# Optimization experiments

Hardware: AMD Instinct MI355X
Metric: run time of the kernel (lower is better)

Reference implementation:

```python
import jax, jax.numpy as jnp
import numpy as np

DIMS = 1024
HEADS = 16
HEAD_DIM = DIMS // HEADS


def setup_inputs() -> dict:
    key = jax.random.key(0)
    k_x, k_q, k_k, k_v = jax.random.split(key, 4)
    scale = 1.0 / np.sqrt(DIMS)
    return {
        "input_seq_embs": jax.random.normal(k_x, (4, 4096, DIMS), dtype=jnp.float32),
        # torch nn.Linear weights have shape (out_features, in_features)
        "W_Q": jax.random.normal(k_q, (DIMS, DIMS), dtype=jnp.float32) * scale,
        "W_K": jax.random.normal(k_k, (DIMS, DIMS), dtype=jnp.float32) * scale,
        "W_V": jax.random.normal(k_v, (DIMS, DIMS), dtype=jnp.float32) * scale,
    }


def reference(input_seq_embs, W_Q, W_K, W_V):
    B, L, d = input_seq_embs.shape
    H, hd = HEADS, HEAD_DIM
    # torch Linear: y = x @ W.T
    Q = (input_seq_embs @ W_Q.T).reshape(B, L, H, hd)
    K = (input_seq_embs @ W_K.T).reshape(B, L, H, hd)
    V = (input_seq_embs @ W_V.T).reshape(B, L, H, hd)
    # NOTE: original code does NOT move heads to dim 1, so matmuls act on
    # the trailing (H, hd) axes per token.
    # softmax(K^T) over heads axis: (B, L, hd, H)
    sK = jax.nn.softmax(jnp.swapaxes(K, -1, -2), axis=-1)
    # tran_V: (B, L, hd, hd)
    tran_V = jnp.einsum("bldh,blhe->blde", sK, V)
    # softmax(Q) over head_dim axis, then (B, L, H, hd)
    out = jnp.einsum("blhd,blde->blhe", jax.nn.softmax(Q, axis=-1), tran_V)
    return out.reshape(B, L, d)
```

## Files before the change

### kernel.cpp

```cpp
#include <hip/hip_runtime.h>
#include <stdint.h>
#include <stddef.h>

#define TOKENS 16384
#define CHUNK  8192
#define DMODEL 1024

typedef short   short8 __attribute__((ext_vector_type(8)));
typedef _Float16 half8 __attribute__((ext_vector_type(8)));
typedef float   f32x4  __attribute__((ext_vector_type(4)));
typedef unsigned short ushort_t;
typedef unsigned short us4 __attribute__((ext_vector_type(4)));

__device__ inline ushort_t f2h(float f) {
  union { _Float16 h; ushort_t u; } x; x.h = (_Float16)f; return x.u;
}
__device__ inline float h2f(ushort_t u) {
  union { _Float16 h; ushort_t u; } x; x.u = u; return (float)x.h;
}

template <typename V>
__device__ auto mfma16h_(V a, V b, f32x4 c, int)
    -> decltype(__builtin_amdgcn_mfma_f32_16x16x32_f16(a, b, c, 0, 0, 0)) {
  return __builtin_amdgcn_mfma_f32_16x16x32_f16(a, b, c, 0, 0, 0);
}
template <typename V>
__device__ f32x4 mfma16h_(V a, V b, f32x4 c, long) {
  return __builtin_amdgcn_mfma_f32_16x16x32_f16(
      __builtin_bit_cast(half8, a), __builtin_bit_cast(half8, b), c, 0, 0, 0);
}
__device__ inline f32x4 MFMA16H(short8 a, short8 b, f32x4 c) {
  return mfma16h_(a, b, c, 0);
}

__device__ inline void gload_lds16(const void* g, void* l) {
  __builtin_amdgcn_global_load_lds(
      (const __attribute__((address_space(1))) unsigned int*)g,
      (__attribute__((address_space(3))) unsigned int*)l, 16, 0, 0);
}

__device__ inline void wave_lds_fence() {
  asm volatile("s_waitcnt lgkmcnt(0)" ::: "memory");
  __builtin_amdgcn_sched_barrier(0);
}

__global__ __launch_bounds__(256) void conv_w(
    const float* __restrict__ Wq, const float* __restrict__ Wk,
    const float* __restrict__ Wv, ushort_t* __restrict__ Wh, int n4)
{
  int i = blockIdx.x * 256 + threadIdx.x;
  if (i >= n4) return;
  const float* src = (blockIdx.y == 0) ? Wq : ((blockIdx.y == 1) ? Wk : Wv);
  f32x4 x = ((const f32x4*)src)[i];
  us4 h;
  #pragma unroll
  for (int j = 0; j < 4; ++j) h[j] = f2h(x[j]);
  ((us4*)(Wh + (size_t)blockIdx.y * DMODEL * DMODEL))[i] = h;
}

__global__ __launch_bounds__(256) void conv_x(
    const float* __restrict__ src, ushort_t* __restrict__ dst, int n4)
{
  int i = blockIdx.x * 256 + threadIdx.x;
  if (i >= n4) return;
  f32x4 x = ((const f32x4*)src)[i];
  us4 h;
  #pragma unroll
  for (int j = 0; j < 4; ++j) h[j] = f2h(x[j]);
  ((us4*)dst)[i] = h;
}

__global__ __launch_bounds__(512, 2) void gemm_h(
    const ushort_t* __restrict__ Xh, const ushort_t* __restrict__ Wh,
    ushort_t* __restrict__ Y, int tokens)
{
  __shared__ ushort_t As[2][256 * 64];
  __shared__ ushort_t Bs[2][256 * 64];

  const int tid  = threadIdx.x;
  const int lane = tid & 63;
  const int wid  = tid >> 6;
  const int quad = lane >> 4;
  const int l15  = lane & 15;
  const int wm   = wid >> 2;
  const int wn   = wid & 3;

  const int m0 = blockIdx.x * 256;
  const int n0 = blockIdx.y * 256;
  const int z  = blockIdx.z;

  const ushort_t* Ag = Xh + (size_t)m0 * DMODEL;
  const ushort_t* Bg = Wh + (size_t)z * DMODEL * DMODEL + (size_t)n0 * DMODEL;
  ushort_t* Yp = Y + (size_t)z * tokens * DMODEL;

  f32x4 acc[8][4] = {};

  auto stageA = [&](int t, int b) {
    const int kbase = t * 64;
    #pragma unroll
    for (int i = 0; i < 4; ++i) {
      const int c    = i * 512 + tid;
      const int row  = c >> 3;
      const int koff = (((c & 7) ^ (row & 7)) << 3);
      gload_lds16(Ag + (size_t)row * DMODEL + kbase + koff,
                  (char*)As[b] + (i * 512 + wid * 64) * 16);
    }
  };
  auto stageB = [&](int t, int b) {
    const int kbase = t * 64;
    #pragma unroll
    for (int i = 0; i < 4; ++i) {
      const int c    = i * 512 + tid;
      const int row  = c >> 3;
      const int koff = (((c & 7) ^ (row & 7)) << 3);
      gload_lds16(Bg + (size_t)row * DMODEL + kbase + koff,
                  (char*)Bs[b] + (i * 512 + wid * 64) * 16);
    }
  };

  stageA(0, 0);
  stageB(0, 0);
  asm volatile("s_waitcnt vmcnt(0)" ::: "memory");
  __syncthreads();

  for (int t = 0; t < DMODEL / 64; ++t) {
    const int b  = t & 1;
    const bool pf = (t + 1 < DMODEL / 64);
    const short8* Av = (const short8*)As[b];
    const short8* Bv = (const short8*)Bs[b];

    short8 bh[4][2];
    #pragma unroll
    for (int j = 0; j < 4; ++j) {
      const int r = wn * 64 + j * 16 + l15;
      #pragma unroll
      for (int s = 0; s < 2; ++s)
        bh[j][s] = Bv[r * 8 + ((s * 4 + quad) ^ (r & 7))];
    }

    #pragma unroll
    for (int p = 0; p < 4; ++p) {
      short8 ah[2][2];
      #pragma unroll
      for (int ii = 0; ii < 2; ++ii) {
        const int r = wm * 128 + (2 * p + ii) * 16 + l15;
        #pragma unroll
        for (int s = 0; s < 2; ++s)
          ah[ii][s] = Av[r * 8 + ((s * 4 + quad) ^ (r & 7))];
      }
      if (p == 0 && pf) stageA(t + 1, b ^ 1);
      if (p == 1 && pf) stageB(t + 1, b ^ 1);

      __builtin_amdgcn_s_barrier();
      asm volatile("s_waitcnt lgkmcnt(0)" ::: "memory");
      __builtin_amdgcn_sched_barrier(0);
      __builtin_amdgcn_s_setprio(1);
      #pragma unroll
      for (int s = 0; s < 2; ++s) {
        #pragma unroll
        for (int ii = 0; ii < 2; ++ii) {
          #pragma unroll
          for (int j = 0; j < 4; ++j)
            acc[2 * p + ii][j] = MFMA16H(ah[ii][s], bh[j][s], acc[2 * p + ii][j]);
        }
      }
      __builtin_amdgcn_s_setprio(0);
      __builtin_amdgcn_s_barrier();
    }

    if (pf) { asm volatile("s_waitcnt vmcnt(0)" ::: "memory"); }
    __syncthreads();
  }

  #pragma unroll
  for (int i = 0; i < 8; ++i) {
    #pragma unroll
    for (int j = 0; j < 4; ++j) {
      #pragma unroll
      for (int r = 0; r < 4; ++r) {
        int row = m0 + wm * 128 + i * 16 + quad * 4 + r;
        int col = n0 + wn * 64 + j * 16 + l15;
        Yp[(size_t)row * DMODEL + col] = f2h(acc[i][j][r]);
      }
    }
  }
}

__global__ __launch_bounds__(256) void attn_mix(
    const ushort_t* __restrict__ QKV, float* __restrict__ Out, int tokens)
{
  __shared__ __align__(16) ushort_t V_s[4][16 * 72];
  __shared__ __align__(16) float    M_s[4][16 * 20];

  const int tid  = threadIdx.x;
  const int lane = tid & 63;
  const int wv   = tid >> 6;
  const int tok  = blockIdx.x * 4 + wv;

  const int l15  = lane & 15;
  const int quad = lane >> 4;
  const int hrow = lane >> 3;
  const int dcol = (lane & 7) * 8;

  ushort_t* Vl = V_s[wv];
  float*    Ml = M_s[wv];

  const size_t base = (size_t)tok * DMODEL;
  const size_t zstr = (size_t)tokens * DMODEL;
  const short8* Q8 = (const short8*)(QKV + base);
  const short8* K8 = (const short8*)(QKV + zstr + base);
  const short8* V8 = (const short8*)(QKV + 2 * zstr + base);

  short8 vra = V8[lane], vrb = V8[64 + lane];
  *(short8*)(Vl + hrow * 72 + dcol)       = vra;
  *(short8*)(Vl + (hrow + 8) * 72 + dcol) = vrb;

  const int fidx = l15 * 8 + quad;
  short8 qf0 = Q8[fidx], qf1 = Q8[fidx + 4];
  short8 kf0 = K8[fidx], kf1 = K8[fidx + 4];

  float eq0[8], eq1[8], ek0[8], ek1[8];
  #pragma unroll
  for (int j = 0; j < 8; ++j) {
    eq0[j] = __expf(h2f((ushort_t)qf0[j]));
    eq1[j] = __expf(h2f((ushort_t)qf1[j]));
    ek0[j] = __expf(h2f((ushort_t)kf0[j]));
    ek1[j] = __expf(h2f((ushort_t)kf1[j]));
  }

  float s0[8], s1[8];
  #pragma unroll
  for (int j = 0; j < 8; ++j) { s0[j] = ek0[j]; s1[j] = ek1[j]; }
  #pragma unroll
  for (int j = 0; j < 8; ++j) {
    s0[j] += __shfl_xor(s0[j], 1);
    s0[j] += __shfl_xor(s0[j], 2);
    s0[j] += __shfl_xor(s0[j], 4);
    s0[j] += __shfl_xor(s0[j], 8);
    s1[j] += __shfl_xor(s1[j], 1);
    s1[j] += __shfl_xor(s1[j], 2);
    s1[j] += __shfl_xor(s1[j], 4);
    s1[j] += __shfl_xor(s1[j], 8);
  }

  float sq = 0.f;
  #pragma unroll
  for (int j = 0; j < 8; ++j) sq += eq0[j] + eq1[j];
  sq += __shfl_xor(sq, 16);
  sq += __shfl_xor(sq, 32);
  const float invSq = __builtin_amdgcn_rcpf(sq);

  short8 a0v, a1v, b0v, b1v;
  #pragma unroll
  for (int j = 0; j < 8; ++j) {
    a0v[j] = (short)f2h(eq0[j] * (invSq * __builtin_amdgcn_rcpf(s0[j])));
    a1v[j] = (short)f2h(eq1[j] * (invSq * __builtin_amdgcn_rcpf(s1[j])));
    b0v[j] = (short)f2h(ek0[j]);
    b1v[j] = (short)f2h(ek1[j]);
  }

  f32x4 acc = {};
  acc = MFMA16H(a0v, b0v, acc);
  acc = MFMA16H(a1v, b1v, acc);

  #pragma unroll
  for (int r = 0; r < 4; ++r) Ml[(quad * 4 + r) * 20 + l15] = acc[r];

  wave_lds_fence();

  f32x4 m0[4], m1[4];
  #pragma unroll
  for (int j = 0; j < 4; ++j) {
    m0[j] = *(const f32x4*)(Ml + hrow * 20 + j * 4);
    m1[j] = *(const f32x4*)(Ml + (hrow + 8) * 20 + j * 4);
  }
  float o0[8] = {0.f, 0.f, 0.f, 0.f, 0.f, 0.f, 0.f, 0.f};
  float o1[8] = {0.f, 0.f, 0.f, 0.f, 0.f, 0.f, 0.f, 0.f};
  #pragma unroll
  for (int hp = 0; hp < 16; ++hp) {
    short8 vv = *(const short8*)(Vl + hp * 72 + dcol);
    const float w0 = m0[hp >> 2][hp & 3];
    const float w1 = m1[hp >> 2][hp & 3];
    #pragma unroll
    for (int j = 0; j < 8; ++j) {
      float vf = h2f((ushort_t)vv[j]);
      o0[j] += w0 * vf;
      o1[j] += w1 * vf;
    }
  }

  float* O0 = Out + base + hrow * 64 + dcol;
  float* O1 = Out + base + (hrow + 8) * 64 + dcol;
  f32x4 w;
  w[0] = o0[0]; w[1] = o0[1]; w[2] = o0[2]; w[3] = o0[3]; *(f32x4*)(O0)     = w;
  w[0] = o0[4]; w[1] = o0[5]; w[2] = o0[6]; w[3] = o0[7]; *(f32x4*)(O0 + 4) = w;
  w[0] = o1[0]; w[1] = o1[1]; w[2] = o1[2]; w[3] = o1[3]; *(f32x4*)(O1)     = w;
  w[0] = o1[4]; w[1] = o1[5]; w[2] = o1[6]; w[3] = o1[7]; *(f32x4*)(O1 + 4) = w;
}

extern "C" void kernel_launch(void* const* d_in, const int* in_sizes, int n_in,
                              void* d_out, int out_size, void* d_ws, size_t ws_size,
                              hipStream_t stream) {
  const float* X  = (const float*)d_in[0];
  const float* Wq = (const float*)d_in[1];
  const float* Wk = (const float*)d_in[2];
  const float* Wv = (const float*)d_in[3];
  float* Out = (float*)d_out;

  const size_t WSZ = (size_t)DMODEL * DMODEL;

  const size_t need1 = (3 * WSZ + (size_t)TOKENS * DMODEL * 4) * sizeof(ushort_t);
  const int    nck  = (ws_size >= need1) ? 1 : 2;
  const size_t ctok = (nck == 1) ? (size_t)TOKENS : (size_t)CHUNK;

  ushort_t* Wh = (ushort_t*)d_ws;
  ushort_t* Xh = Wh + 3 * WSZ;
  ushort_t* Yw = Xh + ctok * DMODEL;

  const int wn4 = (int)(WSZ / 4);
  dim3 gw((wn4 + 255) / 256, 3);
  conv_w<<<gw, 256, 0, stream>>>(Wq, Wk, Wv, Wh, wn4);

  const int xn4 = (int)(ctok * DMODEL / 4);
  dim3 gg((unsigned)(ctok / 256), DMODEL / 256, 3);
  for (int c = 0; c < nck; ++c) {
    conv_x<<<(xn4 + 255) / 256, 256, 0, stream>>>(X + c * ctok * DMODEL, Xh, xn4);
    gemm_h<<<gg, 512, 0, stream>>>(Xh, Wh, Yw, (int)ctok);
    attn_mix<<<(unsigned)(ctok / 4), 256, 0, stream>>>(Yw, Out + c * ctok * DMODEL, (int)ctok);
  }
}
```

Baseline: 262.9 us.

## Pre-swizzle weights into MFMA fragment layout and load B directly to registers

The weight conversion kernel now writes fp16 weights in a layout that matches the MFMA B-fragment ordering per lane. The GEMM drops the B tile from shared memory and has each wave load its B fragments straight from global memory into registers, double-buffered across k-steps. This halves the LDS footprint and removes B's LDS reads and writes. In exchange, each of the two waves sharing a column slice fetches the same B data from global memory or cache, and register pressure rises.

```diff
diff --git a/kernel.cpp b/kernel.cpp
--- a/kernel.cpp
+++ b/kernel.cpp
@@ -44,18 +44,29 @@
   __builtin_amdgcn_sched_barrier(0);
 }
 
-__global__ __launch_bounds__(256) void conv_w(
+__global__ __launch_bounds__(256) void conv_wf(
     const float* __restrict__ Wq, const float* __restrict__ Wk,
-    const float* __restrict__ Wv, ushort_t* __restrict__ Wh, int n4)
+    const float* __restrict__ Wv, ushort_t* __restrict__ Wf)
 {
-  int i = blockIdx.x * 256 + threadIdx.x;
-  if (i >= n4) return;
-  const float* src = (blockIdx.y == 0) ? Wq : ((blockIdx.y == 1) ? Wk : Wv);
-  f32x4 x = ((const f32x4*)src)[i];
-  us4 h;
-  #pragma unroll
-  for (int j = 0; j < 4; ++j) h[j] = f2h(x[j]);
-  ((us4*)(Wh + (size_t)blockIdx.y * DMODEL * DMODEL))[i] = h;
+  const int z = blockIdx.y;
+  const int c = blockIdx.x * 256 + threadIdx.x;
+  const float* src = (z == 0) ? Wq : ((z == 1) ? Wk : Wv);
+  const int lane = c & 63;
+  const int s    = (c >> 6) & 1;
+  const int t    = (c >> 7) & 15;
+  const int G    = c >> 11;
+  const int row  = G * 16 + (lane & 15);
+  const int k    = t * 64 + s * 32 + (lane >> 4) * 8;
+  const float* sp = src + (size_t)row * DMODEL + k;
+  f32x4 a = *(const f32x4*)sp;
+  f32x4 b = *(const f32x4*)(sp + 4);
+  short8 h;
+  #pragma unroll
+  for (int j = 0; j < 4; ++j) {
+    h[j]     = (short)f2h(a[j]);
+    h[4 + j] = (short)f2h(b[j]);
+  }
+  *(short8*)(Wf + (size_t)z * DMODEL * DMODEL + (size_t)c * 8) = h;
 }
 
 __global__ __launch_bounds__(256) void conv_x(
@@ -71,11 +82,10 @@
 }
 
 __global__ __launch_bounds__(512, 2) void gemm_h(
-    const ushort_t* __restrict__ Xh, const ushort_t* __restrict__ Wh,
+    const ushort_t* __restrict__ Xh, const ushort_t* __restrict__ Wf,
     ushort_t* __restrict__ Y, int tokens)
 {
   __shared__ ushort_t As[2][256 * 64];
-  __shared__ ushort_t Bs[2][256 * 64];
 
   const int tid  = threadIdx.x;
   const int lane = tid & 63;
@@ -85,12 +95,12 @@
   const int wm   = wid >> 2;
   const int wn   = wid & 3;
 
-  const int m0 = blockIdx.x * 256;
-  const int n0 = blockIdx.y * 256;
-  const int z  = blockIdx.z;
+  const int m0   = blockIdx.x * 256;
+  const int by16 = blockIdx.y * 16;
+  const int z    = blockIdx.z;
 
   const ushort_t* Ag = Xh + (size_t)m0 * DMODEL;
-  const ushort_t* Bg = Wh + (size_t)z * DMODEL * DMODEL + (size_t)n0 * DMODEL;
+  const ushort_t* Bf = Wf + (size_t)z * DMODEL * DMODEL;
   ushort_t* Yp = Y + (size_t)z * tokens * DMODEL;
 
   f32x4 acc[8][4] = {};
@@ -106,37 +116,27 @@
                   (char*)As[b] + (i * 512 + wid * 64) * 16);
     }
   };
-  auto stageB = [&](int t, int b) {
-    const int kbase = t * 64;
-    #pragma unroll
-    for (int i = 0; i < 4; ++i) {
-      const int c    = i * 512 + tid;
-      const int row  = c >> 3;
-      const int koff = (((c & 7) ^ (row & 7)) << 3);
-      gload_lds16(Bg + (size_t)row * DMODEL + kbase + koff,
-                  (char*)Bs[b] + (i * 512 + wid * 64) * 16);
-    }
+  auto ldB_lo = [&](int t, short8 (&dst)[4][2]) {
+    #pragma unroll
+    for (int j = 0; j < 2; ++j)
+      #pragma unroll
+      for (int s = 0; s < 2; ++s)
+        dst[j][s] = *(const short8*)(
+            Bf + ((((size_t)(by16 + wn * 4 + j) * 16 + t) * 2 + s) << 9) + lane * 8);
   };
-
-  stageA(0, 0);
-  stageB(0, 0);
-  asm volatile("s_waitcnt vmcnt(0)" ::: "memory");
-  __syncthreads();
-
-  for (int t = 0; t < DMODEL / 64; ++t) {
-    const int b  = t & 1;
+  auto ldB_hi = [&](int t, short8 (&dst)[4][2]) {
+    #pragma unroll
+    for (int j = 2; j < 4; ++j)
+      #pragma unroll
+      for (int s = 0; s < 2; ++s)
+        dst[j][s] = *(const short8*)(
+            Bf + ((((size_t)(by16 + wn * 4 + j) * 16 + t) * 2 + s) << 9) + lane * 8);
+  };
+
+  auto body = [&](int t, short8 (&cur)[4][2], short8 (&nxt)[4][2]) {
+    const int b   = t & 1;
     const bool pf = (t + 1 < DMODEL / 64);
     const short8* Av = (const short8*)As[b];
-    const short8* Bv = (const short8*)Bs[b];
-
-    short8 bh[4][2];
-    #pragma unroll
-    for (int j = 0; j < 4; ++j) {
-      const int r = wn * 64 + j * 16 + l15;
-      #pragma unroll
-      for (int s = 0; s < 2; ++s)
-        bh[j][s] = Bv[r * 8 + ((s * 4 + quad) ^ (r & 7))];
-    }
 
     #pragma unroll
     for (int p = 0; p < 4; ++p) {
@@ -148,8 +148,8 @@
         for (int s = 0; s < 2; ++s)
           ah[ii][s] = Av[r * 8 + ((s * 4 + quad) ^ (r & 7))];
       }
-      if (p == 0 && pf) stageA(t + 1, b ^ 1);
-      if (p == 1 && pf) stageB(t + 1, b ^ 1);
+      if (p == 0 && pf) { stageA(t + 1, b ^ 1); ldB_lo(t + 1, nxt); }
+      if (p == 1 && pf) { ldB_hi(t + 1, nxt); }
 
       __builtin_amdgcn_s_barrier();
       asm volatile("s_waitcnt lgkmcnt(0)" ::: "memory");
@@ -161,7 +161,7 @@
         for (int ii = 0; ii < 2; ++ii) {
           #pragma unroll
           for (int j = 0; j < 4; ++j)
-            acc[2 * p + ii][j] = MFMA16H(ah[ii][s], bh[j][s], acc[2 * p + ii][j]);
+            acc[2 * p + ii][j] = MFMA16H(ah[ii][s], cur[j][s], acc[2 * p + ii][j]);
         }
       }
       __builtin_amdgcn_s_setprio(0);
@@ -170,6 +170,18 @@
 
     if (pf) { asm volatile("s_waitcnt vmcnt(0)" ::: "memory"); }
     __syncthreads();
+  };
+
+  short8 bA[4][2], bB[4][2];
+  stageA(0, 0);
+  ldB_lo(0, bA);
+  ldB_hi(0, bA);
+  asm volatile("s_waitcnt vmcnt(0)" ::: "memory");
+  __syncthreads();
+
+  for (int tt = 0; tt < DMODEL / 64; tt += 2) {
+    body(tt, bA, bB);
+    body(tt + 1, bB, bA);
   }
 
   #pragma unroll
@@ -179,7 +191,7 @@
       #pragma unroll
       for (int r = 0; r < 4; ++r) {
         int row = m0 + wm * 128 + i * 16 + quad * 4 + r;
-        int col = n0 + wn * 64 + j * 16 + l15;
+        int col = blockIdx.y * 256 + wn * 64 + j * 16 + l15;
         Yp[(size_t)row * DMODEL + col] = f2h(acc[i][j][r]);
       }
     }
@@ -313,19 +325,18 @@
   const int    nck  = (ws_size >= need1) ? 1 : 2;
   const size_t ctok = (nck == 1) ? (size_t)TOKENS : (size_t)CHUNK;
 
-  ushort_t* Wh = (ushort_t*)d_ws;
-  ushort_t* Xh = Wh + 3 * WSZ;
+  ushort_t* Wf = (ushort_t*)d_ws;
+  ushort_t* Xh = Wf + 3 * WSZ;
   ushort_t* Yw = Xh + ctok * DMODEL;
 
-  const int wn4 = (int)(WSZ / 4);
-  dim3 gw((wn4 + 255) / 256, 3);
-  conv_w<<<gw, 256, 0, stream>>>(Wq, Wk, Wv, Wh, wn4);
+  dim3 gw(512, 3);
+  conv_wf<<<gw, 256, 0, stream>>>(Wq, Wk, Wv, Wf);
 
   const int xn4 = (int)(ctok * DMODEL / 4);
   dim3 gg((unsigned)(ctok / 256), DMODEL / 256, 3);
   for (int c = 0; c < nck; ++c) {
     conv_x<<<(xn4 + 255) / 256, 256, 0, stream>>>(X + c * ctok * DMODEL, Xh, xn4);
-    gemm_h<<<gg, 512, 0, stream>>>(Xh, Wh, Yw, (int)ctok);
+    gemm_h<<<gg, 512, 0, stream>>>(Xh, Wf, Yw, (int)ctok);
     attn_mix<<<(unsigned)(ctok / 4), 256, 0, stream>>>(Yw, Out + c * ctok * DMODEL, (int)ctok);
   }
 }
```

After: 261.8 us. No clear change (-0.4%).
